# Performance work log

Hardware: AMD Instinct MI355X
Metric: run time of the kernel (lower is better)

The kernel has to match this reference:

```python
import jax, jax.numpy as jnp
import numpy as np

EPS = 0.0  # GINConv eps

def _gin_conv(x, edge_index, W1, b1, W2, b2, n_nodes):
    # GINConv: mlp((1+eps)*x + sum_{j in N(i)} x_j)
    src, dst = edge_index[0], edge_index[1]
    agg = jax.ops.segment_sum(x[src], dst, num_segments=n_nodes)  # [N, d]
    h = (1.0 + EPS) * x + agg
    h = jax.nn.relu(h @ W1 + b1)  # Linear -> Identity(BN off) -> ReLU
    return h @ W2 + b2            # second Linear


def setup_inputs() -> dict:
    key = jax.random.key(0)
    ks = jax.random.split(key, 10)
    N, E = 50000, 600000
    d_in, d_hid, d_out = 128, 256, 128
    x = jax.random.normal(ks[0], (N, d_in), dtype=jnp.float32)
    edge_index = jax.random.randint(ks[1], (2, E), 0, N, dtype=jnp.int64)

    def lin(k, fan_in, fan_out):
        bound = 1.0 / np.sqrt(fan_in)
        kw, kb = jax.random.split(k)
        W = jax.random.uniform(kw, (fan_in, fan_out), jnp.float32, -bound, bound)
        b = jax.random.uniform(kb, (fan_out,), jnp.float32, -bound, bound)
        return W, b

    W1a, b1a = lin(ks[2], d_in, d_hid)   # conv0 mlp: 128->256
    W2a, b2a = lin(ks[3], d_hid, d_hid)  # conv0 mlp: 256->256
    W1b, b1b = lin(ks[4], d_hid, d_hid)  # conv1 mlp: 256->256
    W2b, b2b = lin(ks[5], d_hid, d_out)  # conv1 mlp: 256->128
    return {"x": x, "W1a": W1a, "b1a": b1a, "W2a": W2a, "b2a": b2a,
            "W1b": W1b, "b1b": b1b, "W2b": W2b, "b2b": b2b,
            "edge_index": edge_index}


def reference(x, W1a, b1a, W2a, b2a, W1b, b1b, W2b, b2b, edge_index):
    n_nodes = x.shape[0]
    # layer 0: GINConv -> relu (use_bn=False; dropout is identity in eval)
    h = _gin_conv(x, edge_index, W1a, b1a, W2a, b2a, n_nodes)
    h = jax.nn.relu(h)
    # final GINConv (no activation after, per forward())
    return _gin_conv(h, edge_index, W1b, b1b, W2b, b2b, n_nodes)
```

## Files before the change

### kernel.cpp

```cpp
#include <hip/hip_runtime.h>


typedef __bf16 bf16x8 __attribute__((ext_vector_type(8)));
typedef float f32x4 __attribute__((ext_vector_type(4)));
typedef float f32x2 __attribute__((ext_vector_type(2)));
typedef unsigned short u16x4 __attribute__((ext_vector_type(4)));
typedef unsigned short u16x8 __attribute__((ext_vector_type(8)));
typedef unsigned int uint32;
typedef uint32 u32x4 __attribute__((ext_vector_type(4)));

#define MAXDEG 48

__device__ __forceinline__ unsigned short f2bf(float f) {
  uint32 u = __builtin_bit_cast(uint32, f);
  u += 0x7FFFu + ((u >> 16) & 1u);
  return (unsigned short)(u >> 16);
}
__device__ __forceinline__ f32x2 bfpair(uint32 w) {
  f32x2 r;
  r.x = __builtin_bit_cast(float, w << 16);
  r.y = __builtin_bit_cast(float, w & 0xFFFF0000u);
  return r;
}

#define G2L16(gp, lp)                                                        \
  __builtin_amdgcn_global_load_lds(                                          \
      (const __attribute__((address_space(1))) void*)(gp),                   \
      (__attribute__((address_space(3))) void*)(lp), 16, 0, 0)

#define BARRIER()                                                            \
  do {                                                                       \
    asm volatile("" ::: "memory");                                           \
    __builtin_amdgcn_s_barrier();                                            \
    asm volatile("" ::: "memory");                                           \
  } while (0)
#define VMCNT0() asm volatile("s_waitcnt vmcnt(0)" ::: "memory")

__global__ __launch_bounds__(256) void prep_fill(
    const int* __restrict__ eidx, int* __restrict__ deg, int* __restrict__ ell,
    int E, int FB,
    const float* __restrict__ x, unsigned short* __restrict__ xb, long long n4,
    const float* __restrict__ W1a, const float* __restrict__ W2a,
    const float* __restrict__ W1b, const float* __restrict__ W2b,
    unsigned short* __restrict__ w1t, unsigned short* __restrict__ w2t,
    unsigned short* __restrict__ w3t, unsigned short* __restrict__ w4t) {
  int b = blockIdx.x;
  int t = threadIdx.x;
  if (b < FB) {
    int e = b * 256 + t;
    if (e < E) {
      int s = eidx[e];
      int d = eidx[e + E];
      int c = atomicAdd(&deg[d], 1);
      if (c < MAXDEG) ell[d * MAXDEG + c] = s;
    }
  } else if (b < FB + 768) {
    int i = (b - FB) * 256 + t;
    const float* W;
    unsigned short* WT;
    int K, N, j;
    if (i < 32768) {
      W = W1a; WT = w1t; K = 128; N = 256; j = i;
    } else if (i < 98304) {
      W = W2a; WT = w2t; K = 256; N = 256; j = i - 32768;
    } else if (i < 163840) {
      W = W1b; WT = w3t; K = 256; N = 256; j = i - 98304;
    } else {
      W = W2b; WT = w4t; K = 256; N = 128; j = i - 163840;
    }
    int k = j / N, n = j - k * N;
    WT[n * K + k] = f2bf(W[j]);
  } else {
    long long i = (long long)(b - FB - 768) * 256 + t;
    long long stride = (long long)(gridDim.x - FB - 768) * 256;
    for (; i < n4; i += stride) {
      float4 v = ((const float4*)x)[i];
      u16x4 o;
      o.x = f2bf(v.x); o.y = f2bf(v.y); o.z = f2bf(v.z); o.w = f2bf(v.w);
      ((u16x4*)xb)[i] = o;
    }
  }
}

template <int GRP>
__global__ __launch_bounds__(256) void agg_gather(
    unsigned short* __restrict__ out, const unsigned short* __restrict__ src,
    const int* __restrict__ degv, const int* __restrict__ ell, int Nn) {
  constexpr int RS = GRP * 8;
  constexpr int GPB = 256 / GRP;
  const int gid = threadIdx.x / GRP;
  const int gl  = threadIdx.x % GRP;
  const unsigned short* sp = src + gl * 8;
  const int stride = gridDim.x * GPB;
  for (int node = blockIdx.x * GPB + gid; node < Nn; node += stride) {
    const int beg = node * MAXDEG;
    int deg = degv[node];
    if (deg > MAXDEG) deg = MAXDEG;
    f32x2 acc[4];
    {
      u32x4 w = *(const u32x4*)(sp + (size_t)node * RS);
#pragma unroll
      for (int k = 0; k < 4; ++k) acc[k] = bfpair(w[k]);
    }
    int j = 0;
    for (; j + 8 <= deg; j += 8) {
      int idx[8];
#pragma unroll
      for (int u = 0; u < 8; ++u) idx[u] = ell[beg + j + u];
#pragma unroll
      for (int u = 0; u < 8; ++u) {
        u32x4 w = *(const u32x4*)(sp + (size_t)idx[u] * RS);
#pragma unroll
        for (int k = 0; k < 4; ++k) acc[k] += bfpair(w[k]);
      }
    }
    if (j < deg) {
#pragma unroll
      for (int u = 0; u < 8; ++u) {
        int jj = j + u;
        int e = beg + (jj < deg ? jj : deg - 1);
        float sel = (jj < deg) ? 1.f : 0.f;
        f32x2 fs = {sel, sel};
        int rv = ell[e];
        u32x4 w = *(const u32x4*)(sp + (size_t)rv * RS);
#pragma unroll
        for (int k = 0; k < 4; ++k) acc[k] += bfpair(w[k]) * fs;
      }
    }
    u16x8 o;
#pragma unroll
    for (int k = 0; k < 4; ++k) {
      o[2 * k] = f2bf(acc[k].x);
      o[2 * k + 1] = f2bf(acc[k].y);
    }
    *(u16x8*)(out + (size_t)node * RS + gl * 8) = o;
  }
}

template <int K1, int N2, bool OUT_BF16>
__global__ __launch_bounds__(512) void fused_mlp8(
    const unsigned short* __restrict__ A,
    const unsigned short* __restrict__ BT1, const float* __restrict__ b1,
    const unsigned short* __restrict__ BT2, const float* __restrict__ b2,
    void* __restrict__ Cout, int M) {
  __shared__ unsigned short As[2][64 * 32];
  __shared__ unsigned short Bs[2][256 * 32];
  __shared__ unsigned short Ts[64 * 264];
  const int tid = threadIdx.x;
  const int wave = tid >> 6, lane = tid & 63;
  const int quad = lane >> 4, l16 = lane & 15;
  const int rowBase = blockIdx.x * 64;

#define STAGE1(buf, kk)                                                      \
  for (int c = tid; c < 1280; c += 512) {                                    \
    if (c < 256) {                                                           \
      int r = rowBase + (c >> 2);                                            \
      if (r > M - 1) r = M - 1;                                              \
      G2L16(A + (long long)r * K1 + (kk) + (c & 3) * 8, As[buf] + c * 8);    \
    } else {                                                                 \
      int bb = c - 256;                                                      \
      G2L16(BT1 + (long long)(bb >> 2) * K1 + (kk) + (bb & 3) * 8,           \
            Bs[buf] + bb * 8);                                               \
    }                                                                        \
  }

  constexpr int nk1 = K1 / 32;
  f32x4 acc[4][2] = {};
  int cur = 0;
  STAGE1(0, 0);
  VMCNT0();
  BARRIER();
  for (int t = 0; t < nk1; ++t) {
    if (t + 1 < nk1) STAGE1(cur ^ 1, (t + 1) * 32);
    bf16x8 af[4], bfr[2];
#pragma unroll
    for (int mi = 0; mi < 4; ++mi)
      af[mi] = *(const bf16x8*)(As[cur] + (mi * 16 + l16) * 32 + quad * 8);
#pragma unroll
    for (int ni = 0; ni < 2; ++ni)
      bfr[ni] = *(const bf16x8*)(Bs[cur] + (wave * 32 + ni * 16 + l16) * 32 + quad * 8);
#pragma unroll
    for (int mi = 0; mi < 4; ++mi)
#pragma unroll
      for (int ni = 0; ni < 2; ++ni)
        acc[mi][ni] = __builtin_amdgcn_mfma_f32_16x16x32_bf16(
            af[mi], bfr[ni], acc[mi][ni], 0, 0, 0);
    VMCNT0();
    BARRIER();
    cur ^= 1;
  }
#pragma unroll
  for (int ni = 0; ni < 2; ++ni) {
    int col = wave * 32 + ni * 16 + l16;
    float bv = b1[col];
#pragma unroll
    for (int mi = 0; mi < 4; ++mi)
#pragma unroll
      for (int r = 0; r < 4; ++r) {
        int row = mi * 16 + quad * 4 + r;
        Ts[row * 264 + col] = f2bf(fmaxf(acc[mi][ni][r] + bv, 0.f));
      }
  }
  __syncthreads();

  constexpr int NW2 = N2 / 8;
  constexpr int NI2 = NW2 / 16;
  constexpr int NCH2 = N2 * 4;

#define STAGE2(buf, kk)                                                      \
  for (int c = tid; c < NCH2; c += 512)                                      \
    G2L16(BT2 + (long long)(c >> 2) * 256 + (kk) + (c & 3) * 8,              \
          Bs[buf] + c * 8);

  f32x4 acc2[4][NI2] = {};
  cur = 0;
  STAGE2(0, 0);
  VMCNT0();
  BARRIER();
  for (int t = 0; t < 8; ++t) {
    int k2 = t * 32;
    if (t + 1 < 8) STAGE2(cur ^ 1, k2 + 32);
    bf16x8 af[4], bfr[NI2];
#pragma unroll
    for (int mi = 0; mi < 4; ++mi)
      af[mi] = *(const bf16x8*)(Ts + (mi * 16 + l16) * 264 + k2 + quad * 8);
#pragma unroll
    for (int ni = 0; ni < NI2; ++ni)
      bfr[ni] = *(const bf16x8*)(Bs[cur] + (wave * NW2 + ni * 16 + l16) * 32 + quad * 8);
#pragma unroll
    for (int mi = 0; mi < 4; ++mi)
#pragma unroll
      for (int ni = 0; ni < NI2; ++ni)
        acc2[mi][ni] = __builtin_amdgcn_mfma_f32_16x16x32_bf16(
            af[mi], bfr[ni], acc2[mi][ni], 0, 0, 0);
    VMCNT0();
    BARRIER();
    cur ^= 1;
  }
#pragma unroll
  for (int ni = 0; ni < NI2; ++ni) {
    int col = wave * NW2 + ni * 16 + l16;
    float bv = b2[col];
#pragma unroll
    for (int mi = 0; mi < 4; ++mi)
#pragma unroll
      for (int r = 0; r < 4; ++r) {
        int row = rowBase + mi * 16 + quad * 4 + r;
        if (row < M) {
          float o = acc2[mi][ni][r] + bv;
          if (OUT_BF16)
            ((unsigned short*)Cout)[(long long)row * N2 + col] = f2bf(fmaxf(o, 0.f));
          else
            ((float*)Cout)[(long long)row * N2 + col] = o;
        }
      }
  }
#undef STAGE1
#undef STAGE2
}

extern "C" void kernel_launch(void* const* d_in, const int* in_sizes, int n_in,
                              void* d_out, int out_size, void* d_ws, size_t ws_size,
                              hipStream_t stream) {
  const float* x   = (const float*)d_in[0];
  const float* W1a = (const float*)d_in[1];
  const float* b1a = (const float*)d_in[2];
  const float* W2a = (const float*)d_in[3];
  const float* b2a = (const float*)d_in[4];
  const float* W1b = (const float*)d_in[5];
  const float* b1b = (const float*)d_in[6];
  const float* W2b = (const float*)d_in[7];
  const float* b2b = (const float*)d_in[8];
  const int*   ei  = (const int*)d_in[9];

  const int Nn = in_sizes[0] / 128;
  const int E  = in_sizes[9] / 2;
  float* out = (float*)d_out;

  unsigned short* h   = (unsigned short*)d_ws;
  unsigned short* g0  = h  + (size_t)Nn * 256;
  unsigned short* g1  = g0 + (size_t)Nn * 128;
  unsigned short* xb  = g1 + (size_t)Nn * 256;
  unsigned short* w1t = xb + (size_t)Nn * 128;
  unsigned short* w2t = w1t + 256 * 128;
  unsigned short* w3t = w2t + 256 * 256;
  unsigned short* w4t = w3t + 256 * 256;
  int* deg  = (int*)(w4t + 128 * 256);
  int* ell  = deg + Nn;

  dim3 blk(256);
  const int FB = (E + 255) / 256;

  hipMemsetAsync(deg, 0, (size_t)Nn * sizeof(int), stream);
  prep_fill<<<FB + 768 + 2048, blk, 0, stream>>>(
      ei, deg, ell, E, FB, x, xb, (long long)Nn * 128 / 4,
      W1a, W2a, W1b, W2b, w1t, w2t, w3t, w4t);

  int mlpBlocks = (Nn + 63) / 64;

  agg_gather<16><<<2048, blk, 0, stream>>>(g0, xb, deg, ell, Nn);
  fused_mlp8<128, 256, true><<<mlpBlocks, dim3(512), 0, stream>>>(
      g0, w1t, b1a, w2t, b2a, h, Nn);
  agg_gather<32><<<2048, blk, 0, stream>>>(g1, h, deg, ell, Nn);
  fused_mlp8<256, 128, false><<<mlpBlocks, dim3(512), 0, stream>>>(
      g1, w3t, b1b, w4t, b2b, out, Nn);
}
```

Measured before the change: 256.3 us.

## Fuse neighbor aggregation into the MLP kernel via shared-memory tiles

Merges the gather-aggregation kernel into the fused MLP kernel. Each 64-row block first gathers and sums neighbor features directly into a shared-memory A tile, then runs both GEMMs from shared memory. This removes the global round-trip of the aggregated buffers and two kernel launches. In exchange the block's gather phase cannot overlap with its own MFMA work, gather parallelism is tied to the MLP block shape (512 threads per 64 rows), and shared memory is reused between the A tile and the hidden activations.

```diff
diff --git a/kernel.cpp b/kernel.cpp
--- a/kernel.cpp
+++ b/kernel.cpp
@@ -82,100 +82,95 @@
   }
 }
 
-template <int GRP>
-__global__ __launch_bounds__(256) void agg_gather(
-    unsigned short* __restrict__ out, const unsigned short* __restrict__ src,
-    const int* __restrict__ degv, const int* __restrict__ ell, int Nn) {
-  constexpr int RS = GRP * 8;
-  constexpr int GPB = 256 / GRP;
-  const int gid = threadIdx.x / GRP;
-  const int gl  = threadIdx.x % GRP;
-  const unsigned short* sp = src + gl * 8;
-  const int stride = gridDim.x * GPB;
-  for (int node = blockIdx.x * GPB + gid; node < Nn; node += stride) {
-    const int beg = node * MAXDEG;
-    int deg = degv[node];
-    if (deg > MAXDEG) deg = MAXDEG;
-    f32x2 acc[4];
-    {
-      u32x4 w = *(const u32x4*)(sp + (size_t)node * RS);
-#pragma unroll
-      for (int k = 0; k < 4; ++k) acc[k] = bfpair(w[k]);
-    }
-    int j = 0;
-    for (; j + 8 <= deg; j += 8) {
-      int idx[8];
-#pragma unroll
-      for (int u = 0; u < 8; ++u) idx[u] = ell[beg + j + u];
-#pragma unroll
-      for (int u = 0; u < 8; ++u) {
-        u32x4 w = *(const u32x4*)(sp + (size_t)idx[u] * RS);
-#pragma unroll
-        for (int k = 0; k < 4; ++k) acc[k] += bfpair(w[k]);
-      }
-    }
-    if (j < deg) {
-#pragma unroll
-      for (int u = 0; u < 8; ++u) {
-        int jj = j + u;
-        int e = beg + (jj < deg ? jj : deg - 1);
-        float sel = (jj < deg) ? 1.f : 0.f;
-        f32x2 fs = {sel, sel};
-        int rv = ell[e];
-        u32x4 w = *(const u32x4*)(sp + (size_t)rv * RS);
-#pragma unroll
-        for (int k = 0; k < 4; ++k) acc[k] += bfpair(w[k]) * fs;
-      }
-    }
-    u16x8 o;
-#pragma unroll
-    for (int k = 0; k < 4; ++k) {
-      o[2 * k] = f2bf(acc[k].x);
-      o[2 * k + 1] = f2bf(acc[k].y);
-    }
-    *(u16x8*)(out + (size_t)node * RS + gl * 8) = o;
-  }
-}
-
 template <int K1, int N2, bool OUT_BF16>
-__global__ __launch_bounds__(512) void fused_mlp8(
-    const unsigned short* __restrict__ A,
+__global__ __launch_bounds__(512) void fused_layer(
+    const unsigned short* __restrict__ src,
+    const int* __restrict__ degv, const int* __restrict__ ell,
     const unsigned short* __restrict__ BT1, const float* __restrict__ b1,
     const unsigned short* __restrict__ BT2, const float* __restrict__ b2,
-    void* __restrict__ Cout, int M) {
-  __shared__ unsigned short As[2][64 * 32];
+    void* __restrict__ Cout, int Nn) {
+  constexpr int GRP = K1 / 8;
+  __shared__ unsigned short Ash[64 * 264];
   __shared__ unsigned short Bs[2][256 * 32];
-  __shared__ unsigned short Ts[64 * 264];
   const int tid = threadIdx.x;
   const int wave = tid >> 6, lane = tid & 63;
   const int quad = lane >> 4, l16 = lane & 15;
   const int rowBase = blockIdx.x * 64;
 
-#define STAGE1(buf, kk)                                                      \
-  for (int c = tid; c < 1280; c += 512) {                                    \
-    if (c < 256) {                                                           \
-      int r = rowBase + (c >> 2);                                            \
-      if (r > M - 1) r = M - 1;                                              \
-      G2L16(A + (long long)r * K1 + (kk) + (c & 3) * 8, As[buf] + c * 8);    \
-    } else {                                                                 \
-      int bb = c - 256;                                                      \
-      G2L16(BT1 + (long long)(bb >> 2) * K1 + (kk) + (bb & 3) * 8,           \
-            Bs[buf] + bb * 8);                                               \
-    }                                                                        \
-  }
+#define STAGE1B(buf, kk)                                                     \
+  for (int c = tid; c < 1024; c += 512)                                      \
+    G2L16(BT1 + (long long)(c >> 2) * K1 + (kk) + (c & 3) * 8,               \
+          Bs[buf] + c * 8);
+#define STAGE2B(buf, kk)                                                     \
+  for (int c = tid; c < N2 * 4; c += 512)                                    \
+    G2L16(BT2 + (long long)(c >> 2) * 256 + (kk) + (c & 3) * 8,              \
+          Bs[buf] + c * 8);
+
+  STAGE1B(0, 0);
+
+  {
+    constexpr int NPG = 64 * GRP / 512;
+    const int gid = tid / GRP, gl = tid % GRP;
+    const unsigned short* sp = src + gl * 8;
+#pragma unroll
+    for (int nn = 0; nn < NPG; ++nn) {
+      const int lrow = gid * NPG + nn;
+      int node = rowBase + lrow;
+      if (node > Nn - 1) node = Nn - 1;
+      const int beg = node * MAXDEG;
+      int deg = degv[node];
+      if (deg > MAXDEG) deg = MAXDEG;
+      f32x2 acc[4];
+      {
+        u32x4 w = *(const u32x4*)(sp + (size_t)node * K1);
+#pragma unroll
+        for (int k = 0; k < 4; ++k) acc[k] = bfpair(w[k]);
+      }
+      int j = 0;
+      for (; j + 8 <= deg; j += 8) {
+        int idx[8];
+#pragma unroll
+        for (int u = 0; u < 8; ++u) idx[u] = ell[beg + j + u];
+#pragma unroll
+        for (int u = 0; u < 8; ++u) {
+          u32x4 w = *(const u32x4*)(sp + (size_t)idx[u] * K1);
+#pragma unroll
+          for (int k = 0; k < 4; ++k) acc[k] += bfpair(w[k]);
+        }
+      }
+      if (j < deg) {
+#pragma unroll
+        for (int u = 0; u < 8; ++u) {
+          int jj = j + u;
+          int e = beg + (jj < deg ? jj : deg - 1);
+          float sel = (jj < deg) ? 1.f : 0.f;
+          f32x2 fs = {sel, sel};
+          int rv = ell[e];
+          u32x4 w = *(const u32x4*)(sp + (size_t)rv * K1);
+#pragma unroll
+          for (int k = 0; k < 4; ++k) acc[k] += bfpair(w[k]) * fs;
+        }
+      }
+      u16x8 o;
+#pragma unroll
+      for (int k = 0; k < 4; ++k) {
+        o[2 * k] = f2bf(acc[k].x);
+        o[2 * k + 1] = f2bf(acc[k].y);
+      }
+      *(u16x8*)(Ash + lrow * 264 + gl * 8) = o;
+    }
+  }
+  __syncthreads();
 
   constexpr int nk1 = K1 / 32;
-  f32x4 acc[4][2] = {};
+  f32x4 acc1[4][2] = {};
   int cur = 0;
-  STAGE1(0, 0);
-  VMCNT0();
-  BARRIER();
   for (int t = 0; t < nk1; ++t) {
-    if (t + 1 < nk1) STAGE1(cur ^ 1, (t + 1) * 32);
+    if (t + 1 < nk1) STAGE1B(cur ^ 1, (t + 1) * 32);
     bf16x8 af[4], bfr[2];
 #pragma unroll
     for (int mi = 0; mi < 4; ++mi)
-      af[mi] = *(const bf16x8*)(As[cur] + (mi * 16 + l16) * 32 + quad * 8);
+      af[mi] = *(const bf16x8*)(Ash + (mi * 16 + l16) * 264 + t * 32 + quad * 8);
 #pragma unroll
     for (int ni = 0; ni < 2; ++ni)
       bfr[ni] = *(const bf16x8*)(Bs[cur] + (wave * 32 + ni * 16 + l16) * 32 + quad * 8);
@@ -183,12 +178,14 @@
     for (int mi = 0; mi < 4; ++mi)
 #pragma unroll
       for (int ni = 0; ni < 2; ++ni)
-        acc[mi][ni] = __builtin_amdgcn_mfma_f32_16x16x32_bf16(
-            af[mi], bfr[ni], acc[mi][ni], 0, 0, 0);
+        acc1[mi][ni] = __builtin_amdgcn_mfma_f32_16x16x32_bf16(
+            af[mi], bfr[ni], acc1[mi][ni], 0, 0, 0);
     VMCNT0();
     BARRIER();
     cur ^= 1;
   }
+
+  STAGE2B(0, 0);
 #pragma unroll
   for (int ni = 0; ni < 2; ++ni) {
     int col = wave * 32 + ni * 16 + l16;
@@ -198,32 +195,22 @@
 #pragma unroll
       for (int r = 0; r < 4; ++r) {
         int row = mi * 16 + quad * 4 + r;
-        Ts[row * 264 + col] = f2bf(fmaxf(acc[mi][ni][r] + bv, 0.f));
+        Ash[row * 264 + col] = f2bf(fmaxf(acc1[mi][ni][r] + bv, 0.f));
       }
   }
   __syncthreads();
 
   constexpr int NW2 = N2 / 8;
   constexpr int NI2 = NW2 / 16;
-  constexpr int NCH2 = N2 * 4;
-
-#define STAGE2(buf, kk)                                                      \
-  for (int c = tid; c < NCH2; c += 512)                                      \
-    G2L16(BT2 + (long long)(c >> 2) * 256 + (kk) + (c & 3) * 8,              \
-          Bs[buf] + c * 8);
-
   f32x4 acc2[4][NI2] = {};
   cur = 0;
-  STAGE2(0, 0);
-  VMCNT0();
-  BARRIER();
   for (int t = 0; t < 8; ++t) {
     int k2 = t * 32;
-    if (t + 1 < 8) STAGE2(cur ^ 1, k2 + 32);
+    if (t + 1 < 8) STAGE2B(cur ^ 1, k2 + 32);
     bf16x8 af[4], bfr[NI2];
 #pragma unroll
     for (int mi = 0; mi < 4; ++mi)
-      af[mi] = *(const bf16x8*)(Ts + (mi * 16 + l16) * 264 + k2 + quad * 8);
+      af[mi] = *(const bf16x8*)(Ash + (mi * 16 + l16) * 264 + k2 + quad * 8);
 #pragma unroll
     for (int ni = 0; ni < NI2; ++ni)
       bfr[ni] = *(const bf16x8*)(Bs[cur] + (wave * NW2 + ni * 16 + l16) * 32 + quad * 8);
@@ -246,7 +233,7 @@
 #pragma unroll
       for (int r = 0; r < 4; ++r) {
         int row = rowBase + mi * 16 + quad * 4 + r;
-        if (row < M) {
+        if (row < Nn) {
           float o = acc2[mi][ni][r] + bv;
           if (OUT_BF16)
             ((unsigned short*)Cout)[(long long)row * N2 + col] = f2bf(fmaxf(o, 0.f));
@@ -255,8 +242,8 @@
         }
       }
   }
-#undef STAGE1
-#undef STAGE2
+#undef STAGE1B
+#undef STAGE2B
 }
 
 extern "C" void kernel_launch(void* const* d_in, const int* in_sizes, int n_in,
@@ -278,9 +265,7 @@
   float* out = (float*)d_out;
 
   unsigned short* h   = (unsigned short*)d_ws;
-  unsigned short* g0  = h  + (size_t)Nn * 256;
-  unsigned short* g1  = g0 + (size_t)Nn * 128;
-  unsigned short* xb  = g1 + (size_t)Nn * 256;
+  unsigned short* xb  = h  + (size_t)Nn * 256;
   unsigned short* w1t = xb + (size_t)Nn * 128;
   unsigned short* w2t = w1t + 256 * 128;
   unsigned short* w3t = w2t + 256 * 256;
@@ -296,12 +281,10 @@
       ei, deg, ell, E, FB, x, xb, (long long)Nn * 128 / 4,
       W1a, W2a, W1b, W2b, w1t, w2t, w3t, w4t);
 
-  int mlpBlocks = (Nn + 63) / 64;
-
-  agg_gather<16><<<2048, blk, 0, stream>>>(g0, xb, deg, ell, Nn);
-  fused_mlp8<128, 256, true><<<mlpBlocks, dim3(512), 0, stream>>>(
-      g0, w1t, b1a, w2t, b2a, h, Nn);
-  agg_gather<32><<<2048, blk, 0, stream>>>(g1, h, deg, ell, Nn);
-  fused_mlp8<256, 128, false><<<mlpBlocks, dim3(512), 0, stream>>>(
-      g1, w3t, b1b, w4t, b2b, out, Nn);
-}
+  int lb = (Nn + 63) / 64;
+
+  fused_layer<128, 256, true><<<lb, dim3(512), 0, stream>>>(
+      xb, deg, ell, w1t, b1a, w2t, b2a, h, Nn);
+  fused_layer<256, 128, false><<<lb, dim3(512), 0, stream>>>(
+      h, deg, ell, w3t, b1b, w4t, b2b, out, Nn);
+}
```

Measured after the change: 250.7 us. -2.2%, faster.

## Fuse layer-1 neighbor gather into the fused MLP kernel via LDS

Applied to the files above, without the earlier changes.

Adds a fused_layer kernel that gathers each 64-node tile's neighbor sum of h straight into shared memory, then runs both MLP GEMMs with MFMA from that tile. It replaces the separate agg_gather<32> launch and the g1 buffer round trip for the second layer. The goal is to drop one launch and the write and re-read of an Nn x 256 bf16 intermediate. The cost is that the irregular gather now runs inside a 512-thread, LDS-heavy block with lower occupancy, so gather latency may be harder to hide. Each node's adjacency list is also capped at MAXDEG entries.

```diff
diff --git a/kernel.cpp b/kernel.cpp
--- a/kernel.cpp
+++ b/kernel.cpp
@@ -259,6 +259,170 @@
 #undef STAGE2
 }
 
+template <int K1, int N2, bool OUT_BF16>
+__global__ __launch_bounds__(512) void fused_layer(
+    const unsigned short* __restrict__ src,
+    const int* __restrict__ degv, const int* __restrict__ ell,
+    const unsigned short* __restrict__ BT1, const float* __restrict__ b1,
+    const unsigned short* __restrict__ BT2, const float* __restrict__ b2,
+    void* __restrict__ Cout, int Nn) {
+  constexpr int GRP = K1 / 8;
+  __shared__ unsigned short Ash[64 * 264];
+  __shared__ unsigned short Bs[2][256 * 32];
+  const int tid = threadIdx.x;
+  const int wave = tid >> 6, lane = tid & 63;
+  const int quad = lane >> 4, l16 = lane & 15;
+  const int rowBase = blockIdx.x * 64;
+
+#define STAGE1B(buf, kk)                                                     \
+  for (int c = tid; c < 1024; c += 512)                                      \
+    G2L16(BT1 + (long long)(c >> 2) * K1 + (kk) + (c & 3) * 8,               \
+          Bs[buf] + c * 8);
+#define STAGE2B(buf, kk)                                                     \
+  for (int c = tid; c < N2 * 4; c += 512)                                    \
+    G2L16(BT2 + (long long)(c >> 2) * 256 + (kk) + (c & 3) * 8,              \
+          Bs[buf] + c * 8);
+
+  STAGE1B(0, 0);
+
+  {
+    constexpr int NPG = 64 * GRP / 512;
+    const int gid = tid / GRP, gl = tid % GRP;
+    const unsigned short* sp = src + gl * 8;
+#pragma unroll
+    for (int nn = 0; nn < NPG; ++nn) {
+      const int lrow = gid * NPG + nn;
+      int node = rowBase + lrow;
+      if (node > Nn - 1) node = Nn - 1;
+      const int beg = node * MAXDEG;
+      int deg = degv[node];
+      if (deg > MAXDEG) deg = MAXDEG;
+      f32x2 acc[4];
+      {
+        u32x4 w = *(const u32x4*)(sp + (size_t)node * K1);
+#pragma unroll
+        for (int k = 0; k < 4; ++k) acc[k] = bfpair(w[k]);
+      }
+      int j = 0;
+      for (; j + 8 <= deg; j += 8) {
+        int idx[8];
+#pragma unroll
+        for (int u = 0; u < 8; ++u) idx[u] = ell[beg + j + u];
+#pragma unroll
+        for (int u = 0; u < 8; ++u) {
+          u32x4 w = *(const u32x4*)(sp + (size_t)idx[u] * K1);
+#pragma unroll
+          for (int k = 0; k < 4; ++k) acc[k] += bfpair(w[k]);
+        }
+      }
+      if (j < deg) {
+#pragma unroll
+        for (int u = 0; u < 8; ++u) {
+          int jj = j + u;
+          int e = beg + (jj < deg ? jj : deg - 1);
+          float sel = (jj < deg) ? 1.f : 0.f;
+          f32x2 fs = {sel, sel};
+          int rv = ell[e];
+          u32x4 w = *(const u32x4*)(sp + (size_t)rv * K1);
+#pragma unroll
+          for (int k = 0; k < 4; ++k) acc[k] += bfpair(w[k]) * fs;
+        }
+      }
+      u16x8 o;
+#pragma unroll
+      for (int k = 0; k < 4; ++k) {
+        o[2 * k] = f2bf(acc[k].x);
+        o[2 * k + 1] = f2bf(acc[k].y);
+      }
+      *(u16x8*)(Ash + lrow * 264 + gl * 8) = o;
+    }
+  }
+  __syncthreads();
+
+  constexpr int nk1 = K1 / 32;
+  f32x4 acc1[4][2] = {};
+  int cur = 0;
+  for (int t = 0; t < nk1; ++t) {
+    if (t + 1 < nk1) STAGE1B(cur ^ 1, (t + 1) * 32);
+    bf16x8 af[4], bfr[2];
+#pragma unroll
+    for (int mi = 0; mi < 4; ++mi)
+      af[mi] = *(const bf16x8*)(Ash + (mi * 16 + l16) * 264 + t * 32 + quad * 8);
+#pragma unroll
+    for (int ni = 0; ni < 2; ++ni)
+      bfr[ni] = *(const bf16x8*)(Bs[cur] + (wave * 32 + ni * 16 + l16) * 32 + quad * 8);
+#pragma unroll
+    for (int mi = 0; mi < 4; ++mi)
+#pragma unroll
+      for (int ni = 0; ni < 2; ++ni)
+        acc1[mi][ni] = __builtin_amdgcn_mfma_f32_16x16x32_bf16(
+            af[mi], bfr[ni], acc1[mi][ni], 0, 0, 0);
+    VMCNT0();
+    BARRIER();
+    cur ^= 1;
+  }
+
+  STAGE2B(0, 0);
+#pragma unroll
+  for (int ni = 0; ni < 2; ++ni) {
+    int col = wave * 32 + ni * 16 + l16;
+    float bv = b1[col];
+#pragma unroll
+    for (int mi = 0; mi < 4; ++mi)
+#pragma unroll
+      for (int r = 0; r < 4; ++r) {
+        int row = mi * 16 + quad * 4 + r;
+        Ash[row * 264 + col] = f2bf(fmaxf(acc1[mi][ni][r] + bv, 0.f));
+      }
+  }
+  __syncthreads();
+
+  constexpr int NW2 = N2 / 8;
+  constexpr int NI2 = NW2 / 16;
+  f32x4 acc2[4][NI2] = {};
+  cur = 0;
+  for (int t = 0; t < 8; ++t) {
+    int k2 = t * 32;
+    if (t + 1 < 8) STAGE2B(cur ^ 1, k2 + 32);
+    bf16x8 af[4], bfr[NI2];
+#pragma unroll
+    for (int mi = 0; mi < 4; ++mi)
+      af[mi] = *(const bf16x8*)(Ash + (mi * 16 + l16) * 264 + k2 + quad * 8);
+#pragma unroll
+    for (int ni = 0; ni < NI2; ++ni)
+      bfr[ni] = *(const bf16x8*)(Bs[cur] + (wave * NW2 + ni * 16 + l16) * 32 + quad * 8);
+#pragma unroll
+    for (int mi = 0; mi < 4; ++mi)
+#pragma unroll
+      for (int ni = 0; ni < NI2; ++ni)
+        acc2[mi][ni] = __builtin_amdgcn_mfma_f32_16x16x32_bf16(
+            af[mi], bfr[ni], acc2[mi][ni], 0, 0, 0);
+    VMCNT0();
+    BARRIER();
+    cur ^= 1;
+  }
+#pragma unroll
+  for (int ni = 0; ni < NI2; ++ni) {
+    int col = wave * NW2 + ni * 16 + l16;
+    float bv = b2[col];
+#pragma unroll
+    for (int mi = 0; mi < 4; ++mi)
+#pragma unroll
+      for (int r = 0; r < 4; ++r) {
+        int row = rowBase + mi * 16 + quad * 4 + r;
+        if (row < Nn) {
+          float o = acc2[mi][ni][r] + bv;
+          if (OUT_BF16)
+            ((unsigned short*)Cout)[(long long)row * N2 + col] = f2bf(fmaxf(o, 0.f));
+          else
+            ((float*)Cout)[(long long)row * N2 + col] = o;
+        }
+      }
+  }
+#undef STAGE1B
+#undef STAGE2B
+}
+
 extern "C" void kernel_launch(void* const* d_in, const int* in_sizes, int n_in,
                               void* d_out, int out_size, void* d_ws, size_t ws_size,
                               hipStream_t stream) {
@@ -279,8 +443,7 @@
 
   unsigned short* h   = (unsigned short*)d_ws;
   unsigned short* g0  = h  + (size_t)Nn * 256;
-  unsigned short* g1  = g0 + (size_t)Nn * 128;
-  unsigned short* xb  = g1 + (size_t)Nn * 256;
+  unsigned short* xb  = g0 + (size_t)Nn * 128;
   unsigned short* w1t = xb + (size_t)Nn * 128;
   unsigned short* w2t = w1t + 256 * 128;
   unsigned short* w3t = w2t + 256 * 256;
@@ -296,12 +459,11 @@
       ei, deg, ell, E, FB, x, xb, (long long)Nn * 128 / 4,
       W1a, W2a, W1b, W2b, w1t, w2t, w3t, w4t);
 
-  int mlpBlocks = (Nn + 63) / 64;
+  int lb = (Nn + 63) / 64;
 
   agg_gather<16><<<2048, blk, 0, stream>>>(g0, xb, deg, ell, Nn);
-  fused_mlp8<128, 256, true><<<mlpBlocks, dim3(512), 0, stream>>>(
+  fused_mlp8<128, 256, true><<<lb, dim3(512), 0, stream>>>(
       g0, w1t, b1a, w2t, b2a, h, Nn);
-  agg_gather<32><<<2048, blk, 0, stream>>>(g1, h, deg, ell, Nn);
-  fused_mlp8<256, 128, false><<<mlpBlocks, dim3(512), 0, stream>>>(
-      g1, w3t, b1b, w4t, b2b, out, Nn);
-}
+  fused_layer<256, 128, false><<<lb, dim3(512), 0, stream>>>(
+      h, deg, ell, w3t, b1b, w4t, b2b, out, Nn);
+}
```

After: 250.2 us (median of 2 runs). 1.02x faster.
